# Optimization experiments

Measured on AMD Instinct MI355X. Metric: run time of the kernel, lower is better.

Reference implementation:

```python
import jax, jax.numpy as jnp
import numpy as np

N = 10000      # nodes
DEG = 32       # avg degree
D_IN = 256     # in_feats
H = 128        # hidden_layers[0] == hidden_layers[2]
K = 3          # hidden_layers[1] = Chebyshev order
D_OUT = 64     # out_feat


def setup_inputs() -> dict:
    key = jax.random.key(0)
    ks = jax.random.split(key, 8)
    x = jax.random.normal(ks[0], (N, D_IN), jnp.float32)
    # sparse binary adjacency built by scattering into a dense [N, N] matrix
    src = jax.random.randint(ks[1], (N * DEG,), 0, N)
    dst = jax.random.randint(ks[2], (N * DEG,), 0, N)
    adj = jnp.zeros((N, N), jnp.float32).at[src, dst].set(1.0)
    init = lambda k, shape, fan: jax.random.normal(k, shape, jnp.float32) / np.sqrt(fan)
    W_in = init(ks[3], (D_IN, H), D_IN)
    b_in = jnp.zeros((H,), jnp.float32)
    W_cheb = init(ks[4], (K * H, H), K * H)   # dgl ChebConv: Linear(k*in, out)
    b_cheb = jnp.zeros((H,), jnp.float32)
    W_out = init(ks[5], (H, D_OUT), H)
    b_out = jnp.zeros((D_OUT,), jnp.float32)
    return dict(x=x, adj=adj, W_in=W_in, b_in=b_in, W_cheb=W_cheb,
                b_cheb=b_cheb, W_out=W_out, b_out=b_out)


def reference(x, adj, W_in, b_in, W_cheb, b_cheb, W_out, b_out):
    n = x.shape[0]
    # graph construction from dense adjacency (eager, like adj.to_dense().nonzero())
    src, dst = jnp.nonzero(adj)
    # symmetric normalization on in-degrees (dgl ChebConv, norm clamped at 1)
    deg = jax.ops.segment_sum(jnp.ones(src.shape[0], jnp.float32), dst, num_segments=n)
    norm = jnp.clip(deg, 1.0) ** -0.5  # [n]
    re_norm = 2.0 / 2.0  # lambda_max = [2] -> re_norm = 1

    def prop(h):
        # D^{-1/2} A D^{-1/2} h : gather at src, scatter-add at dst
        return jax.ops.segment_sum((h * norm[:, None])[src], dst, num_segments=n) * norm[:, None]

    # input linear + relu
    h = jax.nn.relu(x @ W_in + b_in)
    # Chebyshev recursion (dgl ChebConv with lambda_max=2)
    X0 = h
    X1 = -re_norm * prop(X0) + (re_norm - 1.0) * X0
    Xs = [X0, X1]
    Xpp, Xp = X0, X1
    for _ in range(2, K):
        Xi = -2.0 * re_norm * prop(Xp) + 2.0 * (re_norm - 1.0) * Xp - Xpp
        Xs.append(Xi)
        Xpp, Xp = Xp, Xi
    hc = jax.nn.relu(jnp.concatenate(Xs, axis=1) @ W_cheb + b_cheb)  # [n, H]
    return hc @ W_out + b_out  # [n, D_OUT]
```

## Files before the change

kernel.cpp:

```cpp
#include <hip/hip_runtime.h>
#include <hip/hip_bf16.h>
#include <cstdint>
#include <cstddef>

#define NN 10000
#define MAXDEG 128

__global__ __launch_bounds__(256) void zero_cnt(int* __restrict__ cnt) {
    int i = blockIdx.x * 256 + threadIdx.x;
    if (i < NN) cnt[i] = 0;
}

__global__ __launch_bounds__(256) void adj_scan(const float4* __restrict__ adj4,
                                                int total4,
                                                int* __restrict__ cnt,
                                                int* __restrict__ csr) {
    int idx = blockIdx.x * blockDim.x + threadIdx.x;
    int stride = gridDim.x * blockDim.x;
    for (int p = idx; p < total4; p += stride) {
        float4 v = adj4[p];
        if (v.x != 0.f || v.y != 0.f || v.z != 0.f || v.w != 0.f) {
            int lin = p * 4;
            #pragma unroll
            for (int c = 0; c < 4; ++c) {
                float f = (c == 0) ? v.x : (c == 1) ? v.y : (c == 2) ? v.z : v.w;
                if (f != 0.f) {
                    int l = lin + c;
                    int i = l / NN;
                    int j = l - i * NN;
                    int pos = atomicAdd(&cnt[j], 1);
                    if (pos < MAXDEG) csr[j * MAXDEG + pos] = i;
                }
            }
        }
    }
}

__global__ __launch_bounds__(256) void norm_k(const int* __restrict__ cnt,
                                              float* __restrict__ nrm) {
    int i = blockIdx.x * 256 + threadIdx.x;
    if (i < NN) {
        float d = fmaxf((float)cnt[i], 1.0f);
        nrm[i] = 1.0f / sqrtf(d);
    }
}

template<bool SUB>
__global__ __launch_bounds__(256) void prop_k(float* __restrict__ Xcat,
                                              const int* __restrict__ csr,
                                              const int* __restrict__ cnt,
                                              const float* __restrict__ nrm,
                                              int srcOff, int dstOff, float scale) {
    int j = blockIdx.x * 4 + (threadIdx.x >> 6);
    if (j >= NN) return;
    int lane = threadIdx.x & 63;
    int c = lane * 2;
    int cn = min(cnt[j], MAXDEG);
    const int* nb = csr + j * MAXDEG;
    float ax = 0.f, ay = 0.f;
    for (int e = 0; e < cn; ++e) {
        int i = nb[e];
        float w = nrm[i];
        const float2 h = *(const float2*)(Xcat + (size_t)i * 384 + srcOff + c);
        ax = fmaf(w, h.x, ax);
        ay = fmaf(w, h.y, ay);
    }
    float s = scale * nrm[j];
    float rx = s * ax, ry = s * ay;
    if (SUB) {
        const float2 x0 = *(const float2*)(Xcat + (size_t)j * 384 + c);
        rx -= x0.x;
        ry -= x0.y;
    }
    *(float2*)(Xcat + (size_t)j * 384 + dstOff + c) = make_float2(rx, ry);
}

template<int K, int N, bool RELU>
__global__ __launch_bounds__(256) void gemm_bias(const float* __restrict__ A, int lda,
                                                 const float* __restrict__ W,
                                                 const float* __restrict__ bias,
                                                 float* __restrict__ out, int ldo,
                                                 int M) {
    constexpr int BM = 32, KC = 128;
    constexpr int COLS2 = N / 2;
    constexpr int GR = 256 / COLS2;
    constexpr int RPG = BM / GR;
    __shared__ float Wl[KC * N];
    __shared__ float Al[BM * KC];

    int t = threadIdx.x;
    int r0 = blockIdx.x * BM;
    int c2 = t % COLS2;
    int g = t / COLS2;

    float2 acc[RPG];
    #pragma unroll
    for (int i = 0; i < RPG; ++i) acc[i] = make_float2(0.f, 0.f);

    for (int kk = 0; kk < K; kk += KC) {
        __syncthreads();
        #pragma unroll
        for (int i = 0; i < KC * N / 4 / 256; ++i) {
            int idx = t + i * 256;
            ((float4*)Wl)[idx] = ((const float4*)(W + (size_t)kk * N))[idx];
        }
        #pragma unroll
        for (int i = 0; i < BM * KC / 4 / 256; ++i) {
            int idx = t + i * 256;
            int row = idx / (KC / 4);
            int cf = idx % (KC / 4);
            float4 v = make_float4(0.f, 0.f, 0.f, 0.f);
            if (r0 + row < M)
                v = *(const float4*)(A + (size_t)(r0 + row) * lda + kk + cf * 4);
            *(float4*)(Al + row * KC + cf * 4) = v;
        }
        __syncthreads();

        for (int k = 0; k < KC; k += 4) {
            float4 av[RPG];
            #pragma unroll
            for (int rr = 0; rr < RPG; ++rr)
                av[rr] = *(const float4*)(Al + (g * RPG + rr) * KC + k);
            #pragma unroll
            for (int k2 = 0; k2 < 4; ++k2) {
                float2 wv = *(const float2*)(Wl + (k + k2) * N + c2 * 2);
                #pragma unroll
                for (int rr = 0; rr < RPG; ++rr) {
                    float a = (k2 == 0) ? av[rr].x : (k2 == 1) ? av[rr].y
                              : (k2 == 2) ? av[rr].z : av[rr].w;
                    acc[rr].x = fmaf(a, wv.x, acc[rr].x);
                    acc[rr].y = fmaf(a, wv.y, acc[rr].y);
                }
            }
        }
    }

    float2 bv = *(const float2*)(bias + c2 * 2);
    #pragma unroll
    for (int rr = 0; rr < RPG; ++rr) {
        int r = r0 + g * RPG + rr;
        if (r < M) {
            float2 v = acc[rr];
            v.x += bv.x;
            v.y += bv.y;
            if (RELU) { v.x = fmaxf(v.x, 0.f); v.y = fmaxf(v.y, 0.f); }
            *(float2*)(out + (size_t)r * ldo + c2 * 2) = v;
        }
    }
}

extern "C" void kernel_launch(void* const* d_in, const int* in_sizes, int n_in,
                              void* d_out, int out_size, void* d_ws, size_t ws_size,
                              hipStream_t stream) {
    const float* x      = (const float*)d_in[0];
    const float* adj    = (const float*)d_in[1];
    const float* W_in   = (const float*)d_in[2];
    const float* b_in   = (const float*)d_in[3];
    const float* W_cheb = (const float*)d_in[4];
    const float* b_cheb = (const float*)d_in[5];
    const float* W_out  = (const float*)d_in[6];
    const float* b_out  = (const float*)d_in[7];
    float* out = (float*)d_out;

    char* ws = (char*)d_ws;
    int*   cnt  = (int*)(ws + 0);
    float* nrm  = (float*)(ws + 40960);
    int*   csr  = (int*)(ws + 81920);
    float* Xcat = (float*)(ws + 5201920);
    float* hc   = (float*)(ws + 20561920);

    int adj_total = in_sizes[1];

    zero_cnt<<<(NN + 255) / 256, 256, 0, stream>>>(cnt);
    adj_scan<<<2048, 256, 0, stream>>>((const float4*)adj, adj_total / 4, cnt, csr);
    norm_k<<<(NN + 255) / 256, 256, 0, stream>>>(cnt, nrm);

    int gblk = (NN + 31) / 32;
    gemm_bias<256, 128, true><<<gblk, 256, 0, stream>>>(x, 256, W_in, b_in, Xcat, 384, NN);
    prop_k<false><<<(NN + 3) / 4, 256, 0, stream>>>(Xcat, csr, cnt, nrm, 0, 128, -1.0f);
    prop_k<true><<<(NN + 3) / 4, 256, 0, stream>>>(Xcat, csr, cnt, nrm, 128, 256, -2.0f);
    gemm_bias<384, 128, true><<<gblk, 256, 0, stream>>>(Xcat, 384, W_cheb, b_cheb, hc, 128, NN);
    gemm_bias<128, 64, false><<<gblk, 256, 0, stream>>>(hc, 128, W_out, b_out, out, 64, NN);
}
```

Measured before the change: 275.3 us.

## Store features in bf16, fuse cheb and output GEMMs, inline degree normalization

Intermediate Chebyshev feature matrix is stored as bf16 to halve gather and GEMM load traffic, with fp32 accumulation. The Chebyshev linear layer and the output linear layer are fused into one kernel that keeps the hidden tile in shared memory, removing an intermediate buffer round trip and a launch. The norm kernel is removed, with degree normalization computed inline via rsqrt, and the adjacency scan grid is doubled. bf16 storage reduces precision of intermediates, which may affect tolerance.

```diff
diff --git a/kernel.cpp b/kernel.cpp
--- a/kernel.cpp
+++ b/kernel.cpp
@@ -5,6 +5,17 @@
 
 #define NN 10000
 #define MAXDEG 128
+#define LDX 384
+
+__device__ __forceinline__ float bf2f(unsigned short u) {
+    unsigned int x = ((unsigned int)u) << 16;
+    union { unsigned int i; float f; } c; c.i = x; return c.f;
+}
+__device__ __forceinline__ unsigned short f2bf(float f) {
+    union { float f; unsigned int i; } c; c.f = f;
+    unsigned int x = c.i;
+    return (unsigned short)((x + 0x7fffu + ((x >> 16) & 1u)) >> 16);
+}
 
 __global__ __launch_bounds__(256) void zero_cnt(int* __restrict__ cnt) {
     int i = blockIdx.x * 256 + threadIdx.x;
@@ -36,58 +47,45 @@
     }
 }
 
-__global__ __launch_bounds__(256) void norm_k(const int* __restrict__ cnt,
-                                              float* __restrict__ nrm) {
-    int i = blockIdx.x * 256 + threadIdx.x;
-    if (i < NN) {
-        float d = fmaxf((float)cnt[i], 1.0f);
-        nrm[i] = 1.0f / sqrtf(d);
-    }
-}
-
 template<bool SUB>
-__global__ __launch_bounds__(256) void prop_k(float* __restrict__ Xcat,
+__global__ __launch_bounds__(256) void prop_k(unsigned short* __restrict__ X,
                                               const int* __restrict__ csr,
                                               const int* __restrict__ cnt,
-                                              const float* __restrict__ nrm,
                                               int srcOff, int dstOff, float scale) {
     int j = blockIdx.x * 4 + (threadIdx.x >> 6);
     if (j >= NN) return;
     int lane = threadIdx.x & 63;
-    int c = lane * 2;
-    int cn = min(cnt[j], MAXDEG);
+    int cj = cnt[j];
+    int cn = min(cj, MAXDEG);
     const int* nb = csr + j * MAXDEG;
     float ax = 0.f, ay = 0.f;
     for (int e = 0; e < cn; ++e) {
         int i = nb[e];
-        float w = nrm[i];
-        const float2 h = *(const float2*)(Xcat + (size_t)i * 384 + srcOff + c);
-        ax = fmaf(w, h.x, ax);
-        ay = fmaf(w, h.y, ay);
-    }
-    float s = scale * nrm[j];
+        float w = rsqrtf(fmaxf((float)cnt[i], 1.f));
+        uint32_t h2 = *(const uint32_t*)(X + (size_t)i * LDX + srcOff + lane * 2);
+        ax = fmaf(w, bf2f((unsigned short)h2), ax);
+        ay = fmaf(w, bf2f((unsigned short)(h2 >> 16)), ay);
+    }
+    float s = scale * rsqrtf(fmaxf((float)cj, 1.f));
     float rx = s * ax, ry = s * ay;
     if (SUB) {
-        const float2 x0 = *(const float2*)(Xcat + (size_t)j * 384 + c);
-        rx -= x0.x;
-        ry -= x0.y;
-    }
-    *(float2*)(Xcat + (size_t)j * 384 + dstOff + c) = make_float2(rx, ry);
-}
-
-template<int K, int N, bool RELU>
-__global__ __launch_bounds__(256) void gemm_bias(const float* __restrict__ A, int lda,
-                                                 const float* __restrict__ W,
-                                                 const float* __restrict__ bias,
-                                                 float* __restrict__ out, int ldo,
-                                                 int M) {
-    constexpr int BM = 32, KC = 128;
-    constexpr int COLS2 = N / 2;
-    constexpr int GR = 256 / COLS2;
-    constexpr int RPG = BM / GR;
+        uint32_t x0 = *(const uint32_t*)(X + (size_t)j * LDX + lane * 2);
+        rx -= bf2f((unsigned short)x0);
+        ry -= bf2f((unsigned short)(x0 >> 16));
+    }
+    uint32_t o = (uint32_t)f2bf(rx) | ((uint32_t)f2bf(ry) << 16);
+    *(uint32_t*)(X + (size_t)j * LDX + dstOff + lane * 2) = o;
+}
+
+__global__ __launch_bounds__(256) void gemm_in(const float* __restrict__ A,
+                                               const float* __restrict__ W,
+                                               const float* __restrict__ bias,
+                                               unsigned short* __restrict__ Xc,
+                                               int M) {
+    constexpr int K = 256, N = 128, BM = 32, KC = 128;
+    constexpr int COLS2 = N / 2, GR = 256 / COLS2, RPG = BM / GR;
     __shared__ float Wl[KC * N];
     __shared__ float Al[BM * KC];
-
     int t = threadIdx.x;
     int r0 = blockIdx.x * BM;
     int c2 = t % COLS2;
@@ -111,11 +109,10 @@
             int cf = idx % (KC / 4);
             float4 v = make_float4(0.f, 0.f, 0.f, 0.f);
             if (r0 + row < M)
-                v = *(const float4*)(A + (size_t)(r0 + row) * lda + kk + cf * 4);
+                v = *(const float4*)(A + (size_t)(r0 + row) * K + kk + cf * 4);
             *(float4*)(Al + row * KC + cf * 4) = v;
         }
         __syncthreads();
-
         for (int k = 0; k < KC; k += 4) {
             float4 av[RPG];
             #pragma unroll
@@ -134,17 +131,130 @@
             }
         }
     }
-
     float2 bv = *(const float2*)(bias + c2 * 2);
     #pragma unroll
     for (int rr = 0; rr < RPG; ++rr) {
         int r = r0 + g * RPG + rr;
         if (r < M) {
-            float2 v = acc[rr];
-            v.x += bv.x;
-            v.y += bv.y;
-            if (RELU) { v.x = fmaxf(v.x, 0.f); v.y = fmaxf(v.y, 0.f); }
-            *(float2*)(out + (size_t)r * ldo + c2 * 2) = v;
+            float vx = fmaxf(acc[rr].x + bv.x, 0.f);
+            float vy = fmaxf(acc[rr].y + bv.y, 0.f);
+            uint32_t o = (uint32_t)f2bf(vx) | ((uint32_t)f2bf(vy) << 16);
+            *(uint32_t*)(Xc + (size_t)r * LDX + c2 * 2) = o;
+        }
+    }
+}
+
+__global__ __launch_bounds__(256) void gemm_cheb_out(
+        const unsigned short* __restrict__ A,
+        const float* __restrict__ Wc,
+        const float* __restrict__ bc,
+        const float* __restrict__ Wo,
+        const float* __restrict__ bo,
+        float* __restrict__ out,
+        int M) {
+    constexpr int K = 384, N = 128, BM = 32, KC = 128;
+    constexpr int COLS2 = N / 2, GR = 256 / COLS2, RPG = BM / GR;
+    __shared__ float smem[KC * N + BM * KC];
+    float* Wl = smem;
+    float* Al = smem + KC * N;
+    int t = threadIdx.x;
+    int r0 = blockIdx.x * BM;
+    int c2 = t % COLS2;
+    int g = t / COLS2;
+
+    float2 acc[RPG];
+    #pragma unroll
+    for (int i = 0; i < RPG; ++i) acc[i] = make_float2(0.f, 0.f);
+
+    for (int kk = 0; kk < K; kk += KC) {
+        __syncthreads();
+        #pragma unroll
+        for (int i = 0; i < KC * N / 4 / 256; ++i) {
+            int idx = t + i * 256;
+            ((float4*)Wl)[idx] = ((const float4*)(Wc + (size_t)kk * N))[idx];
+        }
+        #pragma unroll
+        for (int i = 0; i < BM * KC / 4 / 256; ++i) {
+            int eidx = (t + i * 256) * 4;
+            int row = eidx / KC;
+            int col = eidx % KC;
+            float4 v = make_float4(0.f, 0.f, 0.f, 0.f);
+            if (r0 + row < M) {
+                uint2 u = *(const uint2*)(A + (size_t)(r0 + row) * LDX + kk + col);
+                v.x = bf2f((unsigned short)u.x);
+                v.y = bf2f((unsigned short)(u.x >> 16));
+                v.z = bf2f((unsigned short)u.y);
+                v.w = bf2f((unsigned short)(u.y >> 16));
+            }
+            *(float4*)(Al + row * KC + col) = v;
+        }
+        __syncthreads();
+        for (int k = 0; k < KC; k += 4) {
+            float4 av[RPG];
+            #pragma unroll
+            for (int rr = 0; rr < RPG; ++rr)
+                av[rr] = *(const float4*)(Al + (g * RPG + rr) * KC + k);
+            #pragma unroll
+            for (int k2 = 0; k2 < 4; ++k2) {
+                float2 wv = *(const float2*)(Wl + (k + k2) * N + c2 * 2);
+                #pragma unroll
+                for (int rr = 0; rr < RPG; ++rr) {
+                    float a = (k2 == 0) ? av[rr].x : (k2 == 1) ? av[rr].y
+                              : (k2 == 2) ? av[rr].z : av[rr].w;
+                    acc[rr].x = fmaf(a, wv.x, acc[rr].x);
+                    acc[rr].y = fmaf(a, wv.y, acc[rr].y);
+                }
+            }
+        }
+    }
+
+    __syncthreads();
+    float* hcL  = smem;
+    float* WoL  = smem + BM * N;
+    float2 bv = *(const float2*)(bc + c2 * 2);
+    #pragma unroll
+    for (int rr = 0; rr < RPG; ++rr) {
+        int row = g * RPG + rr;
+        float vx = fmaxf(acc[rr].x + bv.x, 0.f);
+        float vy = fmaxf(acc[rr].y + bv.y, 0.f);
+        *(float2*)(hcL + row * N + c2 * 2) = make_float2(vx, vy);
+    }
+    #pragma unroll
+    for (int i = 0; i < 128 * 64 / 4 / 256; ++i) {
+        int idx = t + i * 256;
+        ((float4*)WoL)[idx] = ((const float4*)Wo)[idx];
+    }
+    __syncthreads();
+
+    int c32 = t & 31;
+    int g2 = t >> 5;
+    float2 a2[4];
+    #pragma unroll
+    for (int i = 0; i < 4; ++i) a2[i] = make_float2(0.f, 0.f);
+    for (int k = 0; k < 128; k += 4) {
+        float4 hv[4];
+        #pragma unroll
+        for (int rr = 0; rr < 4; ++rr)
+            hv[rr] = *(const float4*)(hcL + (g2 * 4 + rr) * N + k);
+        #pragma unroll
+        for (int k2 = 0; k2 < 4; ++k2) {
+            float2 wv = *(const float2*)(WoL + (k + k2) * 64 + c32 * 2);
+            #pragma unroll
+            for (int rr = 0; rr < 4; ++rr) {
+                float a = (k2 == 0) ? hv[rr].x : (k2 == 1) ? hv[rr].y
+                          : (k2 == 2) ? hv[rr].z : hv[rr].w;
+                a2[rr].x = fmaf(a, wv.x, a2[rr].x);
+                a2[rr].y = fmaf(a, wv.y, a2[rr].y);
+            }
+        }
+    }
+    float2 bov = *(const float2*)(bo + c32 * 2);
+    #pragma unroll
+    for (int rr = 0; rr < 4; ++rr) {
+        int r = r0 + g2 * 4 + rr;
+        if (r < M) {
+            float2 v = make_float2(a2[rr].x + bov.x, a2[rr].y + bov.y);
+            *(float2*)(out + (size_t)r * 64 + c32 * 2) = v;
         }
     }
 }
@@ -163,22 +273,16 @@
     float* out = (float*)d_out;
 
     char* ws = (char*)d_ws;
-    int*   cnt  = (int*)(ws + 0);
-    float* nrm  = (float*)(ws + 40960);
-    int*   csr  = (int*)(ws + 81920);
-    float* Xcat = (float*)(ws + 5201920);
-    float* hc   = (float*)(ws + 20561920);
+    int*            cnt = (int*)(ws + 0);
+    int*            csr = (int*)(ws + 40960);
+    unsigned short* Xc  = (unsigned short*)(ws + 5160960);
 
     int adj_total = in_sizes[1];
 
     zero_cnt<<<(NN + 255) / 256, 256, 0, stream>>>(cnt);
-    adj_scan<<<2048, 256, 0, stream>>>((const float4*)adj, adj_total / 4, cnt, csr);
-    norm_k<<<(NN + 255) / 256, 256, 0, stream>>>(cnt, nrm);
-
-    int gblk = (NN + 31) / 32;
-    gemm_bias<256, 128, true><<<gblk, 256, 0, stream>>>(x, 256, W_in, b_in, Xcat, 384, NN);
-    prop_k<false><<<(NN + 3) / 4, 256, 0, stream>>>(Xcat, csr, cnt, nrm, 0, 128, -1.0f);
-    prop_k<true><<<(NN + 3) / 4, 256, 0, stream>>>(Xcat, csr, cnt, nrm, 128, 256, -2.0f);
-    gemm_bias<384, 128, true><<<gblk, 256, 0, stream>>>(Xcat, 384, W_cheb, b_cheb, hc, 128, NN);
-    gemm_bias<128, 64, false><<<gblk, 256, 0, stream>>>(hc, 128, W_out, b_out, out, 64, NN);
-}
+    adj_scan<<<4096, 256, 0, stream>>>((const float4*)adj, adj_total / 4, cnt, csr);
+    gemm_in<<<(NN + 31) / 32, 256, 0, stream>>>(x, W_in, b_in, Xc, NN);
+    prop_k<false><<<(NN + 3) / 4, 256, 0, stream>>>(Xc, csr, cnt, 0, 128, -1.0f);
+    prop_k<true><<<(NN + 3) / 4, 256, 0, stream>>>(Xc, csr, cnt, 128, 256, -2.0f);
+    gemm_cheb_out<<<(NN + 31) / 32, 256, 0, stream>>>(Xc, W_cheb, b_cheb, W_out, b_out, out, NN);
+}
```

New measurement: 270.3 us. No clear change (-1.8%).
